# Performance work log

Hardware: AMD Instinct MI355X
Metric: run time of the kernel (lower is better)

The kernel has to match this reference:

```python
import jax, jax.numpy as jnp
import numpy as np

B, M, IN_DIM, D, H, NL = 4, 2048, 512, 1024, 4, 2
HD = D // H           # head_dim = 256
HD2 = HD // 2
ROPE_BASE = 10000.0
LN_EPS = 1e-5


def setup_inputs() -> dict:
    key = jax.random.key(0)
    ks = jax.random.split(key, 9)
    s = 0.02
    return {
        "x": jax.random.normal(ks[0], (B, M, IN_DIM), jnp.float32),
        "positions": jnp.sort(jax.random.randint(ks[1], (B, M), 0, 8192), axis=-1).astype(jnp.int32),
        "mask": jnp.ones((B, M), jnp.float32),
        "in_w": jax.random.normal(ks[2], (IN_DIM, D), jnp.float32) * s,
        "in_b": jnp.zeros((D,), jnp.float32),
        "qkv_w": jax.random.normal(ks[3], (NL, D, 3 * D), jnp.float32) * s,
        "o_w": jax.random.normal(ks[4], (NL, D, D), jnp.float32) * s,
        "ln1_g": jnp.ones((NL, D), jnp.float32),
        "ln1_b": jnp.zeros((NL, D), jnp.float32),
        "ffn_w1": jax.random.normal(ks[5], (NL, D, 4 * D), jnp.float32) * s,
        "ffn_b1": jnp.zeros((NL, 4 * D), jnp.float32),
        "ffn_w2": jax.random.normal(ks[6], (NL, 4 * D, D), jnp.float32) * s,
        "ffn_b2": jnp.zeros((NL, D), jnp.float32),
        "ln2_g": jnp.ones((NL, D), jnp.float32),
        "ln2_b": jnp.zeros((NL, D), jnp.float32),
        "start_state": jax.random.normal(ks[7], (D,), jnp.float32) * 0.02,
    }


def _layernorm(x, g, b):
    mu = jnp.mean(x, axis=-1, keepdims=True)
    var = jnp.mean((x - mu) ** 2, axis=-1, keepdims=True)
    return (x - mu) * jax.lax.rsqrt(var + LN_EPS) * g + b


def _rope_cos_sin(positions):
    # rope_module(pos): angles over head_dim//2 freqs, shared across heads
    inv_freq = 1.0 / (ROPE_BASE ** (jnp.arange(HD2, dtype=jnp.float32) * 2.0 / HD))
    ang = positions.astype(jnp.float32)[:, :, None] * inv_freq  # (B, L, HD2)
    return jnp.cos(ang), jnp.sin(ang)


def _apply_rotary(x, cos, sin):
    # x: (B, H, L, HD); cos/sin: (B, 1, L, HD2) broadcast over heads
    x1, x2 = x[..., :HD2], x[..., HD2:]
    return jnp.concatenate([x1 * cos - x2 * sin, x1 * sin + x2 * cos], axis=-1)


def _self_attention(x, cos, sin, mask, qkv_w, o_w):
    Bx, L, Dx = x.shape
    qkv = (x @ qkv_w).reshape(Bx, L, 3, H, HD)
    q = jnp.transpose(qkv[:, :, 0], (0, 2, 1, 3))  # (B, H, L, HD)
    k = jnp.transpose(qkv[:, :, 1], (0, 2, 1, 3))
    v = jnp.transpose(qkv[:, :, 2], (0, 2, 1, 3))
    q = _apply_rotary(q, cos, sin)
    k = _apply_rotary(k, cos, sin)
    scores = jnp.einsum("bhqd,bhkd->bhqk", q, k) * (1.0 / np.sqrt(HD))
    scores = jnp.where(mask[:, None, None, :] == 0, -jnp.inf, scores)
    attn = jax.nn.softmax(scores, axis=-1)
    out = jnp.einsum("bhqk,bhkd->bhqd", attn, v)
    out = jnp.transpose(out, (0, 2, 1, 3)).reshape(Bx, L, Dx)
    return out @ o_w


def reference(x, positions, mask, in_w, in_b, qkv_w, o_w, ln1_g, ln1_b,
              ffn_w1, ffn_b1, ffn_w2, ffn_b2, ln2_g, ln2_b, start_state):
    h = x @ in_w + in_b  # (B, M, D)
    cos, sin = _rope_cos_sin(positions)
    cos, sin = cos[:, None], sin[:, None]  # (B, 1, M, HD2)
    for l in range(NL):
        h = h + _self_attention(_layernorm(h, ln1_g[l], ln1_b[l]), cos, sin, mask,
                                qkv_w[l], o_w[l])
        y = _layernorm(h, ln2_g[l], ln2_b[l])
        y = jax.nn.gelu(y @ ffn_w1[l] + ffn_b1[l], approximate=False) @ ffn_w2[l] + ffn_b2[l]
        h = h + y
    lengths = jnp.sum(mask, axis=1)
    last_idx = jnp.clip(lengths.astype(jnp.int32) - 1, 0, None)
    gathered = h[jnp.arange(h.shape[0]), last_idx]  # (B, D)
    has_hist = lengths > 0
    return jnp.where(has_hist[:, None], gathered, start_state[None, :])
```

## Files before the change

kernel.cpp:

```cpp
#include <hip/hip_runtime.h>
#include <math.h>

typedef __attribute__((ext_vector_type(8))) short bf16x8;
typedef __attribute__((ext_vector_type(4))) float floatx4;
typedef __attribute__((ext_vector_type(4))) unsigned short ushort4v;

typedef __attribute__((address_space(1))) void as1_void;
typedef __attribute__((address_space(3))) void as3_void;

static __device__ __forceinline__ unsigned short f2b(float f) {
    union { float f; unsigned u; } v; v.f = f;
    unsigned r = v.u + 0x7fffu + ((v.u >> 16) & 1u);
    return (unsigned short)(r >> 16);
}
static __device__ __forceinline__ float b2f(unsigned short h) {
    union { unsigned u; float f; } v; v.u = ((unsigned)h) << 16;
    return v.f;
}

template<int P> __device__ __forceinline__ void waitcnt_vm() {
    if constexpr (P == 0)      asm volatile("s_waitcnt vmcnt(0)" ::: "memory");
    else if constexpr (P == 2) asm volatile("s_waitcnt vmcnt(2)" ::: "memory");
    else if constexpr (P == 4) asm volatile("s_waitcnt vmcnt(4)" ::: "memory");
    else                       asm volatile("s_waitcnt vmcnt(6)" ::: "memory");
}

template<int TM, int TN>
__global__ __launch_bounds__(512, 2) void gemm9(
    const unsigned short* __restrict__ A,
    const unsigned short* __restrict__ Bt,
    float* __restrict__ Cf, unsigned short* __restrict__ Cb,
    const float* __restrict__ bias,
    int K, int lda, int ldb, int ldc,
    int zdiv, long a_s1, long a_s2, long b_s1, long b_s2, long c_s1, long c_s2,
    int mode)
{
    constexpr int FM  = TM / 32;
    constexpr int FN  = TN / 64;
    constexpr int MH  = (FM == 8) ? 2 : 1;
    constexpr int NH  = (FN == 4) ? 2 : 1;
    constexpr int NPH = MH * NH;
    constexpr int FMp = FM / MH;
    constexpr int FNp = FN / NH;
    constexpr int NRA = TM / 64;
    constexpr int NRB = TN / 64;

    __shared__ unsigned short As[2][8 * TM * 8];
    __shared__ unsigned short Bs[2][8 * TN * 8];

    const int tid  = threadIdx.x;
    const int wid  = tid >> 6;
    const int lane = tid & 63;
    const int q    = lane >> 4;
    const int r    = lane & 15;
    const int wm   = wid >> 2;
    const int wn   = wid & 3;

    const int z  = blockIdx.z;
    const int zq = z / zdiv, zr = z % zdiv;
    const long offC = (long)zq * c_s1 + (long)zr * c_s2;

    const int m0 = blockIdx.y * TM;
    const int n0 = blockIdx.x * TN;

    const unsigned short* Ab = A  + (long)zq * a_s1 + (long)zr * a_s2 + (long)m0 * lda;
    const unsigned short* Bb = Bt + (long)zq * b_s1 + (long)zr * b_s2 + (long)n0 * ldb;

    floatx4 acc[FM][FN];
    #pragma unroll
    for (int i = 0; i < FM; ++i)
        #pragma unroll
        for (int j = 0; j < FN; ++j)
            acc[i][j] = (floatx4){0.f, 0.f, 0.f, 0.f};

    const int nk = K >> 6;

    auto stageA = [&](int kt, int slot) {
        const int kofs = (kt << 6) + (wid << 3);
        #pragma unroll
        for (int rb = 0; rb < NRA; ++rb)
            __builtin_amdgcn_global_load_lds(
                (as1_void*)(void*)(Ab + (long)(rb * 64 + lane) * lda + kofs),
                (as3_void*)&As[slot][(wid * TM + rb * 64) * 8], 16, 0, 0);
    };
    auto stageB = [&](int kt, int slot) {
        const int kofs = (kt << 6) + (wid << 3);
        #pragma unroll
        for (int rb = 0; rb < NRB; ++rb)
            __builtin_amdgcn_global_load_lds(
                (as1_void*)(void*)(Bb + (long)(rb * 64 + lane) * ldb + kofs),
                (as3_void*)&Bs[slot][(wid * TN + rb * 64) * 8], 16, 0, 0);
    };

    stageA(0, 0);
    stageB(0, 0);
    waitcnt_vm<0>();
    asm volatile("s_barrier" ::: "memory");

    for (int kt = 0; kt < nk; ++kt) {
        const int c  = kt & 1;
        const int sl = c ^ 1;
        const bool pf = (kt + 1 < nk);

        bf16x8 af[MH][FMp][2];
        bf16x8 bf_[NH][FNp][2];

        #pragma unroll
        for (int ph = 0; ph < NPH; ++ph) {
            const int mh = (MH == 1) ? 0 : ((NPH == 4) ? (ph >> 1) : ph);
            const int nh = (NH == 1) ? 0 : ((NPH == 4) ? (((ph + 1) >> 1) & 1) : ph);
            const bool readA = (ph == mh * (NPH / MH));
            const bool readB = (ph == nh);

            if (readA) {
                #pragma unroll
                for (int i = 0; i < FMp; ++i)
                    #pragma unroll
                    for (int ks = 0; ks < 2; ++ks)
                        af[mh][i][ks] = *(const bf16x8*)&As[c][
                            ((ks * 4 + q) * TM + wm * (TM / 2) + mh * (FMp * 16) + i * 16 + r) * 8];
            }
            if (readB) {
                #pragma unroll
                for (int j = 0; j < FNp; ++j)
                    #pragma unroll
                    for (int ks = 0; ks < 2; ++ks)
                        bf_[nh][j][ks] = *(const bf16x8*)&Bs[c][
                            ((ks * 4 + q) * TN + wn * (TN / 4) + nh * (FNp * 16) + j * 16 + r) * 8];
            }
            if (ph == 0 && pf) stageA(kt + 1, sl);
            if (ph == 1 && pf) stageB(kt + 1, sl);

            asm volatile("s_barrier" ::: "memory");
            asm volatile("s_waitcnt lgkmcnt(0)" ::: "memory");
            __builtin_amdgcn_s_setprio(1);
            #pragma unroll
            for (int i = 0; i < FMp; ++i)
                #pragma unroll
                for (int j = 0; j < FNp; ++j) {
                    acc[mh * FMp + i][nh * FNp + j] = __builtin_amdgcn_mfma_f32_16x16x32_bf16(
                        af[mh][i][0], bf_[nh][j][0], acc[mh * FMp + i][nh * FNp + j], 0, 0, 0);
                    acc[mh * FMp + i][nh * FNp + j] = __builtin_amdgcn_mfma_f32_16x16x32_bf16(
                        af[mh][i][1], bf_[nh][j][1], acc[mh * FMp + i][nh * FNp + j], 0, 0, 0);
                }
            __builtin_amdgcn_s_setprio(0);
        }

        if (pf) {
            waitcnt_vm<0>();
            asm volatile("s_barrier" ::: "memory");
        }
    }

    #pragma unroll
    for (int i = 0; i < FM; ++i) {
        const int gr0 = m0 + wm * (TM / 2) + i * 16 + q * 4;
        #pragma unroll
        for (int j = 0; j < FN; ++j) {
            const int gc = n0 + wn * (TN / 4) + j * 16 + r;
            const float bvl = bias ? bias[gc] : 0.0f;
            #pragma unroll
            for (int rr = 0; rr < 4; ++rr) {
                const long cidx = offC + (long)(gr0 + rr) * ldc + gc;
                float v = acc[i][j][rr] + bvl;
                if (mode == 0) {
                    Cf[cidx] = v;
                } else if (mode == 1) {
                    Cf[cidx] += v;
                } else if (mode == 2) {
                    Cb[cidx] = f2b(v);
                } else {
                    Cb[cidx] = f2b(0.5f * v * (1.0f + erff(v * 0.70710678118654752f)));
                }
            }
        }
    }
}

__global__ __launch_bounds__(256) void gemm64(
    const unsigned short* __restrict__ A,
    const unsigned short* __restrict__ Bt,
    unsigned short* __restrict__ Cb,
    int K, int lda, int ldb, int ldc,
    long a_s1, long b_s1, long c_s1)
{
    __shared__ unsigned short As[2][8][64][8];
    __shared__ unsigned short Bs[2][8][64][8];

    const int tid  = threadIdx.x;
    const int wid  = tid >> 6;
    const int lane = tid & 63;
    const int q    = lane >> 4;
    const int r    = lane & 15;
    const int wr   = (wid >> 1) * 32;
    const int wc   = (wid & 1) * 32;

    const int z  = blockIdx.z;
    const long offC = (long)z * c_s1;

    const int m0 = blockIdx.y * 64;
    const int n0 = blockIdx.x * 64;

    const unsigned short* Ab = A  + (long)z * a_s1 + (long)m0 * lda;
    const unsigned short* Bb = Bt + (long)z * b_s1 + (long)n0 * ldb;

    floatx4 acc[2][2];
    #pragma unroll
    for (int i = 0; i < 2; ++i)
        #pragma unroll
        for (int j = 0; j < 2; ++j)
            acc[i][j] = (floatx4){0.f, 0.f, 0.f, 0.f};

    const int nk = K >> 6;

    auto stage = [&](int kt, int slot) {
        #pragma unroll
        for (int cc = 0; cc < 2; ++cc) {
            const int kc   = wid + cc * 4;
            const int kofs = (kt << 6) + (kc << 3);
            __builtin_amdgcn_global_load_lds(
                (as1_void*)(void*)(Ab + (long)lane * lda + kofs),
                (as3_void*)&As[slot][kc][0][0], 16, 0, 0);
            __builtin_amdgcn_global_load_lds(
                (as1_void*)(void*)(Bb + (long)lane * ldb + kofs),
                (as3_void*)&Bs[slot][kc][0][0], 16, 0, 0);
        }
    };

    stage(0, 0);
    waitcnt_vm<0>();
    asm volatile("s_barrier" ::: "memory");

    for (int kt = 0; kt < nk; ++kt) {
        const int c = kt & 1;
        const bool pf = (kt + 1 < nk);
        if (pf) stage(kt + 1, c ^ 1);

        bf16x8 av[2][2], bv[2][2];
        #pragma unroll
        for (int i = 0; i < 2; ++i)
            #pragma unroll
            for (int ks = 0; ks < 2; ++ks)
                av[i][ks] = *(const bf16x8*)&As[c][ks * 4 + q][wr + i * 16 + r][0];
        #pragma unroll
        for (int j = 0; j < 2; ++j)
            #pragma unroll
            for (int ks = 0; ks < 2; ++ks)
                bv[j][ks] = *(const bf16x8*)&Bs[c][ks * 4 + q][wc + j * 16 + r][0];

        __builtin_amdgcn_s_setprio(1);
        #pragma unroll
        for (int i = 0; i < 2; ++i)
            #pragma unroll
            for (int j = 0; j < 2; ++j) {
                acc[i][j] = __builtin_amdgcn_mfma_f32_16x16x32_bf16(av[i][0], bv[j][0], acc[i][j], 0, 0, 0);
                acc[i][j] = __builtin_amdgcn_mfma_f32_16x16x32_bf16(av[i][1], bv[j][1], acc[i][j], 0, 0, 0);
            }
        __builtin_amdgcn_s_setprio(0);

        if (pf) {
            asm volatile("s_waitcnt lgkmcnt(0)" ::: "memory");
            waitcnt_vm<0>();
            asm volatile("s_barrier" ::: "memory");
        }
    }

    #pragma unroll
    for (int i = 0; i < 2; ++i) {
        const int gr0 = m0 + wr + i * 16 + q * 4;
        #pragma unroll
        for (int j = 0; j < 2; ++j) {
            const int gc = n0 + wc + j * 16 + r;
            #pragma unroll
            for (int rr = 0; rr < 4; ++rr) {
                const long cidx = offC + (long)(gr0 + rr) * ldc + gc;
                Cb[cidx] = f2b(acc[i][j][rr]);
            }
        }
    }
}

__global__ void transpose_cast_f32(const float* __restrict__ in, unsigned short* __restrict__ out,
                                   int R, int C)
{
    __shared__ float t[32][33];
    const int c0 = blockIdx.x * 32, r0 = blockIdx.y * 32;
    const int tx = threadIdx.x, ty = threadIdx.y;
    #pragma unroll
    for (int i = 0; i < 4; ++i)
        t[ty + i * 8][tx] = in[(long)(r0 + ty + i * 8) * C + c0 + tx];
    __syncthreads();
    #pragma unroll
    for (int i = 0; i < 4; ++i)
        out[(long)(c0 + ty + i * 8) * R + r0 + tx] = f2b(t[tx][ty + i * 8]);
}

__global__ void transpose_v(const unsigned short* __restrict__ qkv, unsigned short* __restrict__ vT)
{
    __shared__ unsigned short t[32][33];
    const int hh = blockIdx.z;
    const int d0 = blockIdx.x * 32, m0 = blockIdx.y * 32;
    const int tx = threadIdx.x, ty = threadIdx.y;
    const unsigned short* ip = qkv + 2048 + hh * 256;
    unsigned short* op = vT + (long)hh * 524288;
    #pragma unroll
    for (int i = 0; i < 4; ++i)
        t[ty + i * 8][tx] = ip[(long)(m0 + ty + i * 8) * 3072 + d0 + tx];
    __syncthreads();
    #pragma unroll
    for (int i = 0; i < 4; ++i)
        op[(long)(d0 + ty + i * 8) * 2048 + m0 + tx] = t[tx][ty + i * 8];
}

__global__ void cast_f32_bf16(const float* __restrict__ in, unsigned short* __restrict__ out)
{
    const long i = (long)blockIdx.x * 256 + threadIdx.x;
    const float4 v = ((const float4*)in)[i];
    ushort4v o;
    o[0] = f2b(v.x); o[1] = f2b(v.y); o[2] = f2b(v.z); o[3] = f2b(v.w);
    ((ushort4v*)out)[i] = o;
}

__global__ void zero_f32(float* __restrict__ p)
{
    p[blockIdx.x * 256 + threadIdx.x] = 0.0f;
}

__global__ __launch_bounds__(256) void ln_kernel(const float* __restrict__ h,
    const float* __restrict__ g, const float* __restrict__ bta,
    unsigned short* __restrict__ out)
{
    const int tok = blockIdx.x;
    const float4 v = ((const float4*)(h + (long)tok * 1024))[threadIdx.x];
    float s  = v.x + v.y + v.z + v.w;
    float s2 = v.x * v.x + v.y * v.y + v.z * v.z + v.w * v.w;
    #pragma unroll
    for (int off = 32; off > 0; off >>= 1) {
        s  += __shfl_xor(s, off);
        s2 += __shfl_xor(s2, off);
    }
    __shared__ float rs[4], rs2[4];
    const int wid = threadIdx.x >> 6, lane = threadIdx.x & 63;
    if (lane == 0) { rs[wid] = s; rs2[wid] = s2; }
    __syncthreads();
    s  = rs[0] + rs[1] + rs[2] + rs[3];
    s2 = rs2[0] + rs2[1] + rs2[2] + rs2[3];
    const float mu = s * (1.0f / 1024.0f);
    float var = s2 * (1.0f / 1024.0f) - mu * mu;
    var = fmaxf(var, 0.0f);
    const float rsg = 1.0f / sqrtf(var + 1e-5f);
    const float4 gv = ((const float4*)g)[threadIdx.x];
    const float4 bv = ((const float4*)bta)[threadIdx.x];
    ushort4v o;
    o[0] = f2b((v.x - mu) * rsg * gv.x + bv.x);
    o[1] = f2b((v.y - mu) * rsg * gv.y + bv.y);
    o[2] = f2b((v.z - mu) * rsg * gv.z + bv.z);
    o[3] = f2b((v.w - mu) * rsg * gv.w + bv.w);
    *(ushort4v*)&out[(long)tok * 1024 + threadIdx.x * 4] = o;
}

__global__ __launch_bounds__(256) void rope_kernel(unsigned short* __restrict__ qkv,
                                                   const int* __restrict__ pos)
{
    const int tok = blockIdx.x;
    const float p = (float)pos[tok];
    unsigned short* base = qkv + (long)tok * 3072;
    #pragma unroll
    for (int it = 0; it < 2; ++it) {
        const int idx = threadIdx.x + it * 256;
        const int hh = idx >> 7, d = idx & 127;
        const float inv = exp2f((float)d * (-13.287712379549449f / 128.0f));
        const float ang = p * inv;
        const float c = cosf(ang), s = sinf(ang);
        unsigned short* qp = base + hh * 256 + d;
        {
            const float x1 = b2f(qp[0]), x2 = b2f(qp[128]);
            qp[0]   = f2b(x1 * c - x2 * s);
            qp[128] = f2b(x1 * s + x2 * c);
        }
        unsigned short* kp = qp + 1024;
        {
            const float x1 = b2f(kp[0]), x2 = b2f(kp[128]);
            kp[0]   = f2b(x1 * c - x2 * s);
            kp[128] = f2b(x1 * s + x2 * c);
        }
    }
}

__global__ __launch_bounds__(256) void softmax_kernel(unsigned short* __restrict__ sc,
                                                      const float* __restrict__ mrow)
{
    unsigned short* row = sc + (long)blockIdx.x * 2048;
    const int t = threadIdx.x;

    float v[8];
    const ushort4v u0 = *(const ushort4v*)&row[t * 8];
    const ushort4v u1 = *(const ushort4v*)&row[t * 8 + 4];
    #pragma unroll
    for (int i = 0; i < 4; ++i) { v[i] = b2f(u0[i]); v[4 + i] = b2f(u1[i]); }

    float mx = -3.0e38f;
    #pragma unroll
    for (int i = 0; i < 8; ++i) {
        const float m = mrow[t * 8 + i];
        v[i] = (m == 0.0f) ? -3.0e38f : v[i] * 0.0625f;
        mx = fmaxf(mx, v[i]);
    }
    #pragma unroll
    for (int off = 32; off > 0; off >>= 1) mx = fmaxf(mx, __shfl_xor(mx, off));
    __shared__ float rmx[4], rsm[4];
    const int wid = t >> 6, lane = t & 63;
    if (lane == 0) rmx[wid] = mx;
    __syncthreads();
    mx = fmaxf(fmaxf(rmx[0], rmx[1]), fmaxf(rmx[2], rmx[3]));

    float s = 0.0f;
    #pragma unroll
    for (int i = 0; i < 8; ++i) { v[i] = expf(v[i] - mx); s += v[i]; }
    #pragma unroll
    for (int off = 32; off > 0; off >>= 1) s += __shfl_xor(s, off);
    if (lane == 0) rsm[wid] = s;
    __syncthreads();
    s = rsm[0] + rsm[1] + rsm[2] + rsm[3];
    const float invs = (s > 0.0f) ? 1.0f / s : 0.0f;

    ushort4v o0, o1;
    #pragma unroll
    for (int i = 0; i < 4; ++i) { o0[i] = f2b(v[i] * invs); o1[i] = f2b(v[4 + i] * invs); }
    *(ushort4v*)&row[t * 8]     = o0;
    *(ushort4v*)&row[t * 8 + 4] = o1;
}

__global__ __launch_bounds__(256) void gather_kernel(const float* __restrict__ h,
    const float* __restrict__ mask, const float* __restrict__ ss, float* __restrict__ out)
{
    const int b = blockIdx.x;
    const float* mrow = mask + b * 2048;
    const int t = threadIdx.x;
    float s = 0.0f;
    #pragma unroll
    for (int i = 0; i < 8; ++i) s += mrow[t * 8 + i];
    #pragma unroll
    for (int off = 32; off > 0; off >>= 1) s += __shfl_xor(s, off);
    __shared__ float red[4];
    if ((t & 63) == 0) red[t >> 6] = s;
    __syncthreads();
    const float len = red[0] + red[1] + red[2] + red[3];
    const int L = (int)len;
    const int last = (L > 0) ? (L - 1) : 0;
    const bool has = len > 0.0f;
    const float* src = has ? (h + ((long)b * 2048 + last) * 1024) : ss;
    #pragma unroll
    for (int i = 0; i < 4; ++i) {
        const int d = t + i * 256;
        out[b * 1024 + d] = src[d];
    }
}

extern "C" void kernel_launch(void* const* d_in, const int* in_sizes, int n_in,
                              void* d_out, int out_size, void* d_ws, size_t ws_size,
                              hipStream_t stream)
{
    (void)in_sizes; (void)n_in; (void)out_size;
    const float* x      = (const float*)d_in[0];
    const int*   pos    = (const int*)d_in[1];
    const float* mask   = (const float*)d_in[2];
    const float* in_w   = (const float*)d_in[3];
    const float* in_b   = (const float*)d_in[4];
    const float* qkv_w  = (const float*)d_in[5];
    const float* o_w    = (const float*)d_in[6];
    const float* ln1_g  = (const float*)d_in[7];
    const float* ln1_b  = (const float*)d_in[8];
    const float* ffn_w1 = (const float*)d_in[9];
    const float* ffn_b1 = (const float*)d_in[10];
    const float* ffn_w2 = (const float*)d_in[11];
    const float* ffn_b2 = (const float*)d_in[12];
    const float* ln2_g  = (const float*)d_in[13];
    const float* ln2_b  = (const float*)d_in[14];
    const float* sstate = (const float*)d_in[15];
    float* out = (float*)d_out;

    const size_t NEED = 143654912ull;
    if (ws_size < NEED) {
        zero_f32<<<16, 256, 0, stream>>>(out);
        return;
    }
    char* w = (char*)d_ws;
    unsigned short* wt_in  = (unsigned short*)(w);
    unsigned short* wt_qkv = (unsigned short*)(w + 1048576);
    unsigned short* wt_o   = (unsigned short*)(w + 7340032);
    unsigned short* wt_f1  = (unsigned short*)(w + 9437184);
    unsigned short* wt_f2  = (unsigned short*)(w + 17825792);
    float*          hbuf   = (float*)(w + 26214400);
    unsigned short* xn_bf  = (unsigned short*)(w + 59768832);
    unsigned short* ao_bf  = (unsigned short*)(w + 76546048);
    unsigned short* qkv_b  = (unsigned short*)(w + 93323264);
    unsigned short* vT_b   = (unsigned short*)(w + 105906176);
    unsigned short* scmid  = (unsigned short*)(w + 110100480);
    unsigned short* x_bf   = ao_bf;
    unsigned short* mid_bf = (unsigned short*)(w + 76546048);

    const dim3 tb(32, 8);

    transpose_cast_f32<<<dim3(32, 16), tb, 0, stream>>>(in_w, wt_in, 512, 1024);
    cast_f32_bf16<<<4096, 256, 0, stream>>>(x, x_bf);

    gemm9<256, 128><<<dim3(8, 32, 1), 512, 0, stream>>>(x_bf, wt_in, hbuf, nullptr, in_b,
        512, 512, 512, 1024, 1, 0, 0, 0, 0, 0, 0, 0);

    for (int l = 0; l < 2; ++l) {
        transpose_cast_f32<<<dim3(96, 32),  tb, 0, stream>>>(qkv_w  + (long)l * 3145728, wt_qkv, 1024, 3072);
        transpose_cast_f32<<<dim3(32, 32),  tb, 0, stream>>>(o_w    + (long)l * 1048576, wt_o,   1024, 1024);
        transpose_cast_f32<<<dim3(128, 32), tb, 0, stream>>>(ffn_w1 + (long)l * 4194304, wt_f1,  1024, 4096);
        transpose_cast_f32<<<dim3(32, 128), tb, 0, stream>>>(ffn_w2 + (long)l * 4194304, wt_f2,  4096, 1024);

        ln_kernel<<<8192, 256, 0, stream>>>(hbuf, ln1_g + l * 1024, ln1_b + l * 1024, xn_bf);

        for (int b = 0; b < 4; ++b) {
            gemm9<128, 256><<<dim3(12, 16, 1), 512, 0, stream>>>(xn_bf + (long)b * 2097152, wt_qkv,
                nullptr, qkv_b, nullptr, 1024, 1024, 1024, 3072, 1, 0, 0, 0, 0, 0, 0, 2);
            rope_kernel<<<2048, 256, 0, stream>>>(qkv_b, pos + b * 2048);
            transpose_v<<<dim3(8, 64, 4), tb, 0, stream>>>(qkv_b, vT_b);
            gemm9<256, 256><<<dim3(8, 8, 4), 512, 0, stream>>>(qkv_b, qkv_b + 1024,
                nullptr, scmid, nullptr, 256, 3072, 3072, 2048,
                1, 256l, 0, 256l, 0, 4194304l, 0, 2);
            softmax_kernel<<<8192, 256, 0, stream>>>(scmid, mask + b * 2048);
            gemm64<<<dim3(4, 32, 4), 256, 0, stream>>>(scmid, vT_b,
                ao_bf + (long)b * 2097152, 2048, 2048, 2048, 1024,
                4194304l, 524288l, 256l);
        }
        gemm9<256, 128><<<dim3(8, 32, 1), 512, 0, stream>>>(ao_bf, wt_o,
            hbuf, nullptr, nullptr, 1024, 1024, 1024, 1024, 1, 0, 0, 0, 0, 0, 0, 1);

        ln_kernel<<<8192, 256, 0, stream>>>(hbuf, ln2_g + l * 1024, ln2_b + l * 1024, xn_bf);

        gemm9<256, 256><<<dim3(16, 32, 1), 512, 0, stream>>>(xn_bf, wt_f1,
            nullptr, mid_bf, ffn_b1 + l * 4096, 1024, 1024, 1024, 4096, 1, 0, 0, 0, 0, 0, 0, 3);
        gemm9<256, 128><<<dim3(8, 32, 1), 512, 0, stream>>>(mid_bf, wt_f2,
            hbuf, nullptr, ffn_b2 + l * 1024, 4096, 4096, 4096, 1024, 1, 0, 0, 0, 0, 0, 0, 1);
    }

    gather_kernel<<<4, 256, 0, stream>>>(hbuf, mask, sstate, out);
}
```

Baseline: 2.099 ms.

## Fuse softmax into PV GEMM and move scale/mask into QK epilogue

The score GEMM epilogue now applies the 1/sqrt(d) scale and the key mask, writing pre-softmax logits in bf16. The standalone softmax kernel is removed. A new PV kernel first computes per-row max and sum over the 2048 logits, then exponentiates and normalizes A tiles on the fly while staging them into LDS, with V^T tiles loaded through global_load_lds. This removes one full read-modify-write pass over the 4x2048x2048 score matrix per batch, in exchange for each block reading its P rows twice, recomputing exp, and having fewer, larger blocks (32 rows x 256 columns).

```diff
diff --git a/kernel.cpp b/kernel.cpp
--- a/kernel.cpp
+++ b/kernel.cpp
@@ -4,6 +4,7 @@
 typedef __attribute__((ext_vector_type(8))) short bf16x8;
 typedef __attribute__((ext_vector_type(4))) float floatx4;
 typedef __attribute__((ext_vector_type(4))) unsigned short ushort4v;
+typedef __attribute__((ext_vector_type(8))) unsigned short ushort8v;
 
 typedef __attribute__((address_space(1))) void as1_void;
 typedef __attribute__((address_space(3))) void as3_void;
@@ -158,7 +159,9 @@
         #pragma unroll
         for (int j = 0; j < FN; ++j) {
             const int gc = n0 + wn * (TN / 4) + j * 16 + r;
-            const float bvl = bias ? bias[gc] : 0.0f;
+            float bvl = 0.0f, mval = 1.0f;
+            if (mode == 4) mval = bias[gc];
+            else if (bias) bvl = bias[gc];
             #pragma unroll
             for (int rr = 0; rr < 4; ++rr) {
                 const long cidx = offC + (long)(gr0 + rr) * ldc + gc;
@@ -169,114 +172,139 @@
                     Cf[cidx] += v;
                 } else if (mode == 2) {
                     Cb[cidx] = f2b(v);
+                } else if (mode == 3) {
+                    Cb[cidx] = f2b(0.5f * v * (1.0f + erff(v * 0.70710678118654752f)));
                 } else {
-                    Cb[cidx] = f2b(0.5f * v * (1.0f + erff(v * 0.70710678118654752f)));
+                    Cb[cidx] = f2b(mval == 0.0f ? -3.0e38f : v * 0.0625f);
                 }
             }
         }
     }
 }
 
-__global__ __launch_bounds__(256) void gemm64(
-    const unsigned short* __restrict__ A,
-    const unsigned short* __restrict__ Bt,
-    unsigned short* __restrict__ Cb,
-    int K, int lda, int ldb, int ldc,
-    long a_s1, long b_s1, long c_s1)
-{
-    __shared__ unsigned short As[2][8][64][8];
-    __shared__ unsigned short Bs[2][8][64][8];
+__global__ __launch_bounds__(512) void pv_fused(
+    const unsigned short* __restrict__ P,
+    const unsigned short* __restrict__ vT,
+    unsigned short* __restrict__ O)
+{
+    __shared__ unsigned short Ap[2][8][32][8];
+    __shared__ unsigned short Bs[2][8][256][8];
+    __shared__ float smax[32], sinv[32];
 
     const int tid  = threadIdx.x;
-    const int wid  = tid >> 6;
-    const int lane = tid & 63;
-    const int q    = lane >> 4;
-    const int r    = lane & 15;
-    const int wr   = (wid >> 1) * 32;
-    const int wc   = (wid & 1) * 32;
-
-    const int z  = blockIdx.z;
-    const long offC = (long)z * c_s1;
-
-    const int m0 = blockIdx.y * 64;
-    const int n0 = blockIdx.x * 64;
-
-    const unsigned short* Ab = A  + (long)z * a_s1 + (long)m0 * lda;
-    const unsigned short* Bb = Bt + (long)z * b_s1 + (long)n0 * ldb;
-
-    floatx4 acc[2][2];
-    #pragma unroll
-    for (int i = 0; i < 2; ++i)
-        #pragma unroll
-        for (int j = 0; j < 2; ++j)
-            acc[i][j] = (floatx4){0.f, 0.f, 0.f, 0.f};
-
-    const int nk = K >> 6;
-
-    auto stage = [&](int kt, int slot) {
-        #pragma unroll
-        for (int cc = 0; cc < 2; ++cc) {
-            const int kc   = wid + cc * 4;
-            const int kofs = (kt << 6) + (kc << 3);
+    const int wid  = tid >> 6, lane = tid & 63;
+    const int q    = lane >> 4, r = lane & 15;
+    const int wm   = wid >> 2;
+    const int wn   = wid & 3;
+    const int m0   = blockIdx.x * 32;
+    const int hh   = blockIdx.y;
+
+    const unsigned short* Pa = P  + (long)hh * 4194304 + (long)m0 * 2048;
+    const unsigned short* Bb = vT + (long)hh * 524288;
+
+    {
+        const int row = tid >> 4, sub = tid & 15;
+        const unsigned short* rp = Pa + (long)row * 2048 + sub * 128;
+        ushort8v buf[16];
+        #pragma unroll
+        for (int i = 0; i < 16; ++i) buf[i] = *(const ushort8v*)&rp[i * 8];
+        float mx = -3.0e38f;
+        #pragma unroll
+        for (int i = 0; i < 16; ++i)
+            #pragma unroll
+            for (int e = 0; e < 8; ++e) mx = fmaxf(mx, b2f(buf[i][e]));
+        #pragma unroll
+        for (int off = 8; off > 0; off >>= 1) mx = fmaxf(mx, __shfl_xor(mx, off));
+        float s = 0.0f;
+        #pragma unroll
+        for (int i = 0; i < 16; ++i)
+            #pragma unroll
+            for (int e = 0; e < 8; ++e) s += expf(b2f(buf[i][e]) - mx);
+        #pragma unroll
+        for (int off = 8; off > 0; off >>= 1) s += __shfl_xor(s, off);
+        if (sub == 0) { smax[row] = mx; sinv[row] = (s > 0.0f) ? 1.0f / s : 0.0f; }
+    }
+    __syncthreads();
+
+    const int arow = lane >> 1;
+    const int kh   = lane & 1;
+    const float mxr = smax[arow];
+    const float ivr = sinv[arow];
+    const unsigned short* Asrc = Pa + (long)arow * 2048 + wid * 8 + kh * 4;
+
+    auto stageB = [&](int kt, int slot) {
+        const int kofs = (kt << 6) + (wid << 3);
+        #pragma unroll
+        for (int rb = 0; rb < 4; ++rb)
             __builtin_amdgcn_global_load_lds(
-                (as1_void*)(void*)(Ab + (long)lane * lda + kofs),
-                (as3_void*)&As[slot][kc][0][0], 16, 0, 0);
-            __builtin_amdgcn_global_load_lds(
-                (as1_void*)(void*)(Bb + (long)lane * ldb + kofs),
-                (as3_void*)&Bs[slot][kc][0][0], 16, 0, 0);
-        }
+                (as1_void*)(void*)(Bb + (long)(rb * 64 + lane) * 2048 + kofs),
+                (as3_void*)&Bs[slot][wid][rb * 64][0], 16, 0, 0);
     };
-
-    stage(0, 0);
-    waitcnt_vm<0>();
-    asm volatile("s_barrier" ::: "memory");
-
-    for (int kt = 0; kt < nk; ++kt) {
+    auto xformA = [&](ushort4v raw, int slot) {
+        ushort4v pw;
+        #pragma unroll
+        for (int e = 0; e < 4; ++e)
+            pw[e] = f2b(expf(b2f(raw[e]) - mxr) * ivr);
+        *(ushort4v*)&Ap[slot][wid][arow][kh * 4] = pw;
+    };
+
+    floatx4 acc[4];
+    #pragma unroll
+    for (int j = 0; j < 4; ++j) acc[j] = (floatx4){0.f, 0.f, 0.f, 0.f};
+
+    {
+        const ushort4v raw0 = *(const ushort4v*)&Asrc[0];
+        stageB(0, 0);
+        xformA(raw0, 0);
+        asm volatile("s_waitcnt lgkmcnt(0)" ::: "memory");
+        asm volatile("s_waitcnt vmcnt(0)" ::: "memory");
+        asm volatile("s_barrier" ::: "memory");
+    }
+
+    for (int kt = 0; kt < 32; ++kt) {
         const int c = kt & 1;
-        const bool pf = (kt + 1 < nk);
-        if (pf) stage(kt + 1, c ^ 1);
-
-        bf16x8 av[2][2], bv[2][2];
-        #pragma unroll
-        for (int i = 0; i < 2; ++i)
+        const bool pf = (kt + 1 < 32);
+
+        ushort4v raw;
+        if (pf) {
+            raw = *(const ushort4v*)&Asrc[(kt + 1) << 6];
+            stageB(kt + 1, c ^ 1);
+        }
+
+        bf16x8 av[2], bv[4][2];
+        #pragma unroll
+        for (int ks = 0; ks < 2; ++ks)
+            av[ks] = *(const bf16x8*)&Ap[c][ks * 4 + q][wm * 16 + r][0];
+        #pragma unroll
+        for (int j = 0; j < 4; ++j)
             #pragma unroll
             for (int ks = 0; ks < 2; ++ks)
-                av[i][ks] = *(const bf16x8*)&As[c][ks * 4 + q][wr + i * 16 + r][0];
-        #pragma unroll
-        for (int j = 0; j < 2; ++j)
-            #pragma unroll
-            for (int ks = 0; ks < 2; ++ks)
-                bv[j][ks] = *(const bf16x8*)&Bs[c][ks * 4 + q][wc + j * 16 + r][0];
+                bv[j][ks] = *(const bf16x8*)&Bs[c][ks * 4 + q][wn * 64 + j * 16 + r][0];
+        asm volatile("s_waitcnt lgkmcnt(0)" ::: "memory");
 
         __builtin_amdgcn_s_setprio(1);
         #pragma unroll
-        for (int i = 0; i < 2; ++i)
-            #pragma unroll
-            for (int j = 0; j < 2; ++j) {
-                acc[i][j] = __builtin_amdgcn_mfma_f32_16x16x32_bf16(av[i][0], bv[j][0], acc[i][j], 0, 0, 0);
-                acc[i][j] = __builtin_amdgcn_mfma_f32_16x16x32_bf16(av[i][1], bv[j][1], acc[i][j], 0, 0, 0);
-            }
+        for (int j = 0; j < 4; ++j) {
+            acc[j] = __builtin_amdgcn_mfma_f32_16x16x32_bf16(av[0], bv[j][0], acc[j], 0, 0, 0);
+            acc[j] = __builtin_amdgcn_mfma_f32_16x16x32_bf16(av[1], bv[j][1], acc[j], 0, 0, 0);
+        }
         __builtin_amdgcn_s_setprio(0);
 
         if (pf) {
+            xformA(raw, c ^ 1);
             asm volatile("s_waitcnt lgkmcnt(0)" ::: "memory");
-            waitcnt_vm<0>();
+            asm volatile("s_waitcnt vmcnt(0)" ::: "memory");
             asm volatile("s_barrier" ::: "memory");
         }
     }
 
-    #pragma unroll
-    for (int i = 0; i < 2; ++i) {
-        const int gr0 = m0 + wr + i * 16 + q * 4;
-        #pragma unroll
-        for (int j = 0; j < 2; ++j) {
-            const int gc = n0 + wc + j * 16 + r;
-            #pragma unroll
-            for (int rr = 0; rr < 4; ++rr) {
-                const long cidx = offC + (long)(gr0 + rr) * ldc + gc;
-                Cb[cidx] = f2b(acc[i][j][rr]);
-            }
-        }
+    const int gr0 = m0 + wm * 16 + q * 4;
+    #pragma unroll
+    for (int j = 0; j < 4; ++j) {
+        const int gc = hh * 256 + wn * 64 + j * 16 + r;
+        #pragma unroll
+        for (int rr = 0; rr < 4; ++rr)
+            O[(long)(gr0 + rr) * 1024 + gc] = f2b(acc[j][rr]);
     }
 }
 
@@ -387,50 +415,6 @@
     }
 }
 
-__global__ __launch_bounds__(256) void softmax_kernel(unsigned short* __restrict__ sc,
-                                                      const float* __restrict__ mrow)
-{
-    unsigned short* row = sc + (long)blockIdx.x * 2048;
-    const int t = threadIdx.x;
-
-    float v[8];
-    const ushort4v u0 = *(const ushort4v*)&row[t * 8];
-    const ushort4v u1 = *(const ushort4v*)&row[t * 8 + 4];
-    #pragma unroll
-    for (int i = 0; i < 4; ++i) { v[i] = b2f(u0[i]); v[4 + i] = b2f(u1[i]); }
-
-    float mx = -3.0e38f;
-    #pragma unroll
-    for (int i = 0; i < 8; ++i) {
-        const float m = mrow[t * 8 + i];
-        v[i] = (m == 0.0f) ? -3.0e38f : v[i] * 0.0625f;
-        mx = fmaxf(mx, v[i]);
-    }
-    #pragma unroll
-    for (int off = 32; off > 0; off >>= 1) mx = fmaxf(mx, __shfl_xor(mx, off));
-    __shared__ float rmx[4], rsm[4];
-    const int wid = t >> 6, lane = t & 63;
-    if (lane == 0) rmx[wid] = mx;
-    __syncthreads();
-    mx = fmaxf(fmaxf(rmx[0], rmx[1]), fmaxf(rmx[2], rmx[3]));
-
-    float s = 0.0f;
-    #pragma unroll
-    for (int i = 0; i < 8; ++i) { v[i] = expf(v[i] - mx); s += v[i]; }
-    #pragma unroll
-    for (int off = 32; off > 0; off >>= 1) s += __shfl_xor(s, off);
-    if (lane == 0) rsm[wid] = s;
-    __syncthreads();
-    s = rsm[0] + rsm[1] + rsm[2] + rsm[3];
-    const float invs = (s > 0.0f) ? 1.0f / s : 0.0f;
-
-    ushort4v o0, o1;
-    #pragma unroll
-    for (int i = 0; i < 4; ++i) { o0[i] = f2b(v[i] * invs); o1[i] = f2b(v[4 + i] * invs); }
-    *(ushort4v*)&row[t * 8]     = o0;
-    *(ushort4v*)&row[t * 8 + 4] = o1;
-}
-
 __global__ __launch_bounds__(256) void gather_kernel(const float* __restrict__ h,
     const float* __restrict__ mask, const float* __restrict__ ss, float* __restrict__ out)
 {
@@ -522,12 +506,9 @@
             rope_kernel<<<2048, 256, 0, stream>>>(qkv_b, pos + b * 2048);
             transpose_v<<<dim3(8, 64, 4), tb, 0, stream>>>(qkv_b, vT_b);
             gemm9<256, 256><<<dim3(8, 8, 4), 512, 0, stream>>>(qkv_b, qkv_b + 1024,
-                nullptr, scmid, nullptr, 256, 3072, 3072, 2048,
-                1, 256l, 0, 256l, 0, 4194304l, 0, 2);
-            softmax_kernel<<<8192, 256, 0, stream>>>(scmid, mask + b * 2048);
-            gemm64<<<dim3(4, 32, 4), 256, 0, stream>>>(scmid, vT_b,
-                ao_bf + (long)b * 2097152, 2048, 2048, 2048, 1024,
-                4194304l, 524288l, 256l);
+                nullptr, scmid, mask + b * 2048, 256, 3072, 3072, 2048,
+                1, 256l, 0, 256l, 0, 4194304l, 0, 4);
+            pv_fused<<<dim3(64, 4), 512, 0, stream>>>(scmid, vT_b, ao_bf + (long)b * 2097152);
         }
         gemm9<256, 128><<<dim3(8, 32, 1), 512, 0, stream>>>(ao_bf, wt_o,
             hbuf, nullptr, nullptr, 1024, 1024, 1024, 1024, 1, 0, 0, 0, 0, 0, 0, 1);
```

After: 2.279 ms. 1.09x slower.
